# Kernel optimization log

Hardware: AMD Instinct MI355X
Metric: run time of the kernel (lower is better)

The kernel has to match this reference:

```python
import jax, jax.numpy as jnp
import numpy as np


def _rel_coords_log(ws: int) -> np.ndarray:
    # matches torch.meshgrid default indexing='ij'
    idx = np.arange(ws, dtype=np.float32)
    coords = np.stack(np.meshgrid(idx, idx, indexing='ij'), axis=0).reshape(2, -1)  # [2, ws^2]
    rel = coords[:, :, None] - coords[:, None, :]  # [2, T, T]
    rel = rel.transpose(1, 2, 0).reshape(-1, 2)    # [T*T, 2]
    return np.sign(rel) * np.log1p(np.abs(rel))


def setup_inputs() -> dict:
    key = jax.random.key(0)
    ks = jax.random.split(key, 9)
    B, C, Hd, ws, meta_h = 256, 256, 8, 16, 256
    s = 1.0 / np.sqrt(C)
    return {
        'x': jax.random.normal(ks[0], (B, C, ws, ws), dtype=jnp.float32),
        'w_qkv': jax.random.normal(ks[1], (3 * C, C), dtype=jnp.float32) * s,
        'b_qkv': jax.random.normal(ks[2], (3 * C,), dtype=jnp.float32) * 0.01,
        'w_proj': jax.random.normal(ks[3], (C, C), dtype=jnp.float32) * s,
        'b_proj': jax.random.normal(ks[4], (C,), dtype=jnp.float32) * 0.01,
        'mw1': jax.random.normal(ks[5], (meta_h, 2), dtype=jnp.float32) * 0.5,
        'mb1': jax.random.normal(ks[6], (meta_h,), dtype=jnp.float32) * 0.01,
        'mw2': jax.random.normal(ks[7], (Hd, meta_h), dtype=jnp.float32) * (1.0 / np.sqrt(meta_h)),
        'mb2': jax.random.normal(ks[8], (Hd,), dtype=jnp.float32) * 0.01,
        'tau': jnp.ones((1, Hd, 1, 1), dtype=jnp.float32),
    }


def reference(x, w_qkv, b_qkv, w_proj, b_proj, mw1, mb1, mw2, mb2, tau):
    B, C, H, W = x.shape
    T = H * W
    nh = tau.shape[1]
    hd = C // nh
    # [B, C, H, W] -> [B, T, C]
    xt = x.reshape(B, C, T).transpose(0, 2, 1)
    qkv = xt @ w_qkv.T + b_qkv                                  # [B, T, 3C]
    qkv = qkv.reshape(B, T, 3, nh, hd).transpose(2, 0, 3, 1, 4)  # [3, B, nh, T, hd]
    q, k, v = qkv[0], qkv[1], qkv[2]
    # cosine similarity attention
    qn = jnp.linalg.norm(q, axis=-1, keepdims=True)              # [B, nh, T, 1]
    kn = jnp.linalg.norm(k, axis=-1, keepdims=True)
    denom = jnp.maximum(qn * kn.transpose(0, 1, 3, 2), 1e-6)
    scores = jnp.einsum('bhqd,bhkd->bhqk', q, k) / denom
    scores = scores / jnp.maximum(tau, 0.01)
    # MLP relative position bias (static coords)
    rc = jnp.asarray(_rel_coords_log(H))                          # [T*T, 2]
    bias = jax.nn.relu(rc @ mw1.T + mb1) @ mw2.T + mb2            # [T*T, nh]
    bias = bias.T.reshape(nh, T, T)
    scores = scores + bias[None]
    attn = jax.nn.softmax(scores, axis=-1)
    out = jnp.einsum('bhqk,bhkd->bhqd', attn, v)                  # [B, nh, T, hd]
    out = out.transpose(0, 2, 1, 3).reshape(B, T, C)
    out = out @ w_proj.T + b_proj
    return out.transpose(0, 2, 1).reshape(B, C, H, W)
```

## Files before the change

kernel.cpp:

```cpp
#include <hip/hip_runtime.h>
#include <math.h>

#define Cc 256
#define NH 8
#define HD 32
#define Tt 256
#define MH 256
#define TBL 961

typedef _Float16 f16;
typedef f16 f16x4 __attribute__((ext_vector_type(4)));
typedef f16 f16x8 __attribute__((ext_vector_type(8)));
typedef float f32x4 __attribute__((ext_vector_type(4)));

__device__ __forceinline__ f16x8 ld8(const f16* base, int row, int kc) {
  return *(const f16x8*)&base[row * 32 + ((kc ^ ((row >> 2) & 3)) << 3)];
}
__device__ __forceinline__ void st8(f16* base, int row, int kc, f16x8 v) {
  *(f16x8*)&base[row * 32 + ((kc ^ ((row >> 2) & 3)) << 3)] = v;
}
__device__ __forceinline__ int sidx(int row, int col) {
  return row * 32 + (((col >> 3) ^ ((row >> 2) & 3)) << 3) + (col & 7);
}
__device__ __forceinline__ int vsidx(int d, int t) {
  return d * 256 + (((t >> 3) ^ (d & 7)) << 3) + (t & 7);
}
__device__ __forceinline__ f16x8 vld8(const f16* base, int d, int tch) {
  return *(const f16x8*)&base[d * 256 + ((tch ^ (d & 7)) << 3)];
}

__global__ __launch_bounds__(256) void prep_kernel(
    const float* __restrict__ mw1, const float* __restrict__ mb1,
    const float* __restrict__ mw2, const float* __restrict__ mb2,
    const float* __restrict__ w_proj, const float* __restrict__ w_qkv,
    float* __restrict__ table, float* __restrict__ tablemax,
    f16* __restrict__ wpf, f16* __restrict__ wqf) {
  int blk = blockIdx.x, tid = threadIdx.x;
  if (blk >= NH + 32) {
    int blk2 = blk - NH - 32;
#pragma unroll
    for (int pass = 0; pass < 4; pass++) {
      int chunkid = blk2 * 256 + tid + pass * 6144;
      int row = chunkid >> 5, ck = chunkid & 31;
      int hh = row / 96, n = row % 96;
      int srow = ((n >> 5) << 8) + (hh << 5) + (n & 31);
      const float* wp = w_qkv + (size_t)srow * Cc + ck * 8;
      f16x8 v;
#pragma unroll
      for (int u = 0; u < 8; u++) v[u] = (f16)wp[u];
      *(f16x8*)&wqf[(size_t)row * Cc + ck * 8] = v;
    }
    return;
  }
  if (blk >= NH) {
    int base = (blk - NH) * 2048 + tid * 8;
    f16x8 v;
#pragma unroll
    for (int u = 0; u < 8; u++) v[u] = (f16)w_proj[base + u];
    *(f16x8*)&wpf[base] = v;
    return;
  }
  __shared__ float s_w1a[MH], s_w1b[MH], s_b1[MH], s_w2[MH];
  __shared__ float red[256];
  for (int i = tid; i < MH; i += 256) {
    s_w1a[i] = mw1[2 * i];
    s_w1b[i] = mw1[2 * i + 1];
    s_b1[i] = mb1[i];
    s_w2[i] = mw2[blk * MH + i];
  }
  __syncthreads();
  float lmax = -1e30f;
  float b2 = mb2[blk];
  for (int idx = tid; idx < TBL; idx += 256) {
    float fdi = (float)(idx / 31 - 15);
    float fdj = (float)(idx % 31 - 15);
    float d0 = (fdi > 0.f ? 1.f : (fdi < 0.f ? -1.f : 0.f)) * log1pf(fabsf(fdi));
    float d1 = (fdj > 0.f ? 1.f : (fdj < 0.f ? -1.f : 0.f)) * log1pf(fabsf(fdj));
    float o = b2;
    for (int m = 0; m < MH; m++) {
      float hid = fmaxf(fmaf(d0, s_w1a[m], fmaf(d1, s_w1b[m], s_b1[m])), 0.f);
      o = fmaf(hid, s_w2[m], o);
    }
    table[blk * TBL + idx] = o;
    lmax = fmaxf(lmax, o);
  }
  red[tid] = lmax;
  __syncthreads();
  for (int s = 128; s > 0; s >>= 1) {
    if (tid < s) red[tid] = fmaxf(red[tid], red[tid + s]);
    __syncthreads();
  }
  if (tid == 0) tablemax[blk] = red[0];
}

__global__ __launch_bounds__(256) void xpose_kernel(const float* __restrict__ x,
                                                    f16* __restrict__ xt) {
  __shared__ __align__(16) f16 tile[64 * 72];
  int blk = blockIdx.x;
  int b = blk >> 4, ti = (blk >> 2) & 3, tj = blk & 3;
  int tid = threadIdx.x;
  const float* xb = x + (size_t)b * 65536;
  int t4 = (tid & 15) * 4, cg = tid >> 4;
#pragma unroll
  for (int p = 0; p < 4; p++) {
    int cl = cg + p * 16;
    float4 v = *(const float4*)&xb[(size_t)(ti * 64 + cl) * 256 + tj * 64 + t4];
    const float* vp = (const float*)&v;
#pragma unroll
    for (int u = 0; u < 4; u++) {
      int tl = t4 + u;
      tile[tl * 72 + (((cl >> 3) ^ (tl & 7)) << 3) + (cl & 7)] = (f16)vp[u];
    }
  }
  __syncthreads();
  f16* xtb = xt + (size_t)b * 65536;
#pragma unroll
  for (int u = 0; u < 2; u++) {
    int chunk = tid * 2 + u;
    int tr = chunk >> 3, ck = chunk & 7;
    f16x8 v = *(const f16x8*)&tile[tr * 72 + ((ck ^ (tr & 7)) << 3)];
    *(f16x8*)&xtb[(size_t)(tj * 64 + tr) * 256 + ti * 64 + ck * 8] = v;
  }
}

__global__ __launch_bounds__(512, 4) void fused_attn(
    const f16* __restrict__ xt, const f16* __restrict__ wqf,
    const float* __restrict__ b_qkv, const float* __restrict__ table,
    const float* __restrict__ tablemax, const float* __restrict__ tau,
    f16* __restrict__ attnH) {
  __shared__ __align__(16) char smem[68352];
  f16* Qa = (f16*)smem;
  f16* Ka = (f16*)(smem + 16384);
  f16* Vt = (f16*)(smem + 32768);
  f16* Pspare = (f16*)(smem + 49152);
  float* tbv = (float*)(smem + 51456);
  float* rs = (float*)(smem + 67328);
  f16* Xa = (f16*)smem;
  f16* Wa = (f16*)(smem + 16384);

  int tid = threadIdx.x;
  int o = blockIdx.x;
  int bh = ((o & 7) << 8) | (o >> 3);
  int b = bh >> 3, h = bh & 7;
  int wv = tid >> 6, ln = tid & 63, lq = ln >> 4, lm = ln & 15;

  const float LOG2E = 1.4426950408889634f;
  float rtau = 1.0f / fmaxf(tau[h], 0.01f);
  float tmaxh = tablemax[h];

  for (int idx = tid; idx < 31 * 32; idx += 512) {
    int di_ = idx >> 5, c = idx & 31;
    float4 v;
    float* vp = (float*)&v;
#pragma unroll
    for (int u = 0; u < 4; u++) {
      int dj = c - u;
      dj = dj < 0 ? 0 : (dj > 30 ? 30 : dj);
      vp[u] = (table[h * TBL + di_ * 31 + dj] - tmaxh - rtau * 1.0001f) * LOG2E;
    }
    *(float4*)&tbv[idx * 4] = v;
  }

  float bj[6];
#pragma unroll
  for (int nt = 0; nt < 6; nt++) {
    int n = nt * 16 + lm;
    int row = ((n >> 5) << 8) + (h << 5) + (n & 31);
    bj[nt] = b_qkv[row];
  }

  const f16* xtb = xt + (size_t)b * 65536;
  const f16* wqh = wqf + (size_t)h * 24576;
  int xt_ = tid >> 1, xkc = (tid & 1) * 2;
  int wn = tid >> 2, wck = tid & 3;

  f32x4 acc[2][6] = {};
  f16x8 xv0, xv1, wvv;
  xv0 = *(const f16x8*)&xtb[xt_ * 256 + xkc * 8];
  xv1 = *(const f16x8*)&xtb[xt_ * 256 + xkc * 8 + 8];
  if (tid < 384) wvv = *(const f16x8*)&wqh[wn * 256 + wck * 8];

  for (int c0 = 0; c0 < Cc; c0 += 32) {
    st8(Xa, xt_, xkc, xv0);
    st8(Xa, xt_, xkc + 1, xv1);
    if (tid < 384) st8(Wa, wn, wck, wvv);
    __syncthreads();
    if (c0 + 32 < Cc) {
      xv0 = *(const f16x8*)&xtb[xt_ * 256 + c0 + 32 + xkc * 8];
      xv1 = *(const f16x8*)&xtb[xt_ * 256 + c0 + 32 + xkc * 8 + 8];
      if (tid < 384) wvv = *(const f16x8*)&wqh[wn * 256 + c0 + 32 + wck * 8];
    }
    f16x8 af[2], bf[6];
#pragma unroll
    for (int e = 0; e < 2; e++) af[e] = ld8(Xa, wv * 32 + e * 16 + lm, lq);
#pragma unroll
    for (int nt = 0; nt < 6; nt++) bf[nt] = ld8(Wa, nt * 16 + lm, lq);
#pragma unroll
    for (int e = 0; e < 2; e++)
#pragma unroll
      for (int nt = 0; nt < 6; nt++)
        acc[e][nt] = __builtin_amdgcn_mfma_f32_16x16x32_f16(af[e], bf[nt],
                                                            acc[e][nt], 0, 0, 0);
    __syncthreads();
  }

#pragma unroll
  for (int e = 0; e < 2; e++) {
#pragma unroll
    for (int nt = 0; nt < 6; nt++) {
      int d = (nt & 1) * 16 + lm;
#pragma unroll
      for (int r = 0; r < 4; r++) {
        int t = wv * 32 + e * 16 + lq * 4 + r;
        f16 v = (f16)(acc[e][nt][r] + bj[nt]);
        if (nt < 2)      Qa[sidx(t, d)] = v;
        else if (nt < 4) Ka[sidx(t, d)] = v;
        else             Vt[vsidx(d, t)] = v;
      }
    }
  }
  __syncthreads();

  if (tid < 256) {
    int t = tid;
    float s = 0.f;
    f16x8 v[4];
#pragma unroll
    for (int ck = 0; ck < 4; ck++) {
      v[ck] = ld8(Qa, t, ck);
#pragma unroll
      for (int u = 0; u < 8; u++) { float f = (float)v[ck][u]; s = fmaf(f, f, s); }
    }
    float sc_ = rsqrtf(s) * rtau * LOG2E;
#pragma unroll
    for (int ck = 0; ck < 4; ck++) {
      f16x8 o2;
#pragma unroll
      for (int u = 0; u < 8; u++) o2[u] = (f16)((float)v[ck][u] * sc_);
      st8(Qa, t, ck, o2);
    }
  } else {
    int t = tid - 256;
    float s = 0.f;
    f16x8 v[4];
#pragma unroll
    for (int ck = 0; ck < 4; ck++) {
      v[ck] = ld8(Ka, t, ck);
#pragma unroll
      for (int u = 0; u < 8; u++) { float f = (float)v[ck][u]; s = fmaf(f, f, s); }
    }
    float sc_ = rsqrtf(s);
#pragma unroll
    for (int ck = 0; ck < 4; ck++) {
      f16x8 o2;
#pragma unroll
      for (int u = 0; u < 8; u++) o2[u] = (f16)((float)v[ck][u] * sc_);
      st8(Ka, t, ck, o2);
    }
  }
  __syncthreads();

  f16x8 qf[2];
#pragma unroll
  for (int e = 0; e < 2; e++) qf[e] = ld8(Qa, wv * 32 + e * 16 + lm, lq);
  __syncthreads();

  f16* Pme = (wv < 7) ? (Qa + wv * 1152) : Pspare;
  int c0l = lm - lq * 4 + 15;
  const float4* tbp = (const float4*)tbv;
  float lsum[2] = {0.f, 0.f};
  f32x4 acco[2][2] = {};
  int dibase = wv * 2 + 15;

  for (int n0 = 0; n0 < Tt; n0 += 32) {
    f16x8 kf[2];
#pragma unroll
    for (int nt = 0; nt < 2; nt++) kf[nt] = ld8(Ka, n0 + nt * 16 + lm, lq);
    f32x4 zero = {0.f, 0.f, 0.f, 0.f};
    f32x4 sc[2][2];
    __builtin_amdgcn_s_setprio(1);
#pragma unroll
    for (int e = 0; e < 2; e++)
#pragma unroll
      for (int nt = 0; nt < 2; nt++)
        sc[e][nt] = __builtin_amdgcn_mfma_f32_16x16x32_f16(kf[nt], qf[e], zero,
                                                           0, 0, 0);
    __builtin_amdgcn_s_setprio(0);
#pragma unroll
    for (int e = 0; e < 2; e++) {
#pragma unroll
      for (int nt = 0; nt < 2; nt++) {
        int di_ = dibase + e - (n0 >> 4) - nt;
        float4 bv = tbp[di_ * 32 + c0l];
        const float* bvp = (const float*)&bv;
        f16x4 pv;
#pragma unroll
        for (int r = 0; r < 4; r++) {
          float p = exp2f(sc[e][nt][r] + bvp[r]);
          lsum[e] += p;
          pv[r] = (f16)p;
        }
        *(f16x4*)&Pme[(e * 16 + lm) * 36 + nt * 16 + lq * 4] = pv;
      }
    }
    asm volatile("s_waitcnt lgkmcnt(0)" ::: "memory");
    f16x8 pf[2], vf[2];
#pragma unroll
    for (int e = 0; e < 2; e++) {
      f16x4 p0 = *(f16x4*)&Pme[(e * 16 + lm) * 36 + lq * 8];
      f16x4 p1 = *(f16x4*)&Pme[(e * 16 + lm) * 36 + lq * 8 + 4];
      pf[e] = __builtin_shufflevector(p0, p1, 0, 1, 2, 3, 4, 5, 6, 7);
    }
#pragma unroll
    for (int dt = 0; dt < 2; dt++)
      vf[dt] = vld8(Vt, dt * 16 + lm, (n0 >> 3) + lq);
    __builtin_amdgcn_s_setprio(1);
#pragma unroll
    for (int e = 0; e < 2; e++)
#pragma unroll
      for (int dt = 0; dt < 2; dt++)
        acco[e][dt] = __builtin_amdgcn_mfma_f32_16x16x32_f16(pf[e], vf[dt],
                                                             acco[e][dt], 0, 0, 0);
    __builtin_amdgcn_s_setprio(0);
  }

#pragma unroll
  for (int e = 0; e < 2; e++) {
    float v = lsum[e];
    v += __shfl_xor(v, 16);
    v += __shfl_xor(v, 32);
    lsum[e] = v;
  }
  if (ln < 16) {
    rs[wv * 32 + lm] = lsum[0];
    rs[wv * 32 + 16 + lm] = lsum[1];
  }
  asm volatile("s_waitcnt lgkmcnt(0)" ::: "memory");
#pragma unroll
  for (int e = 0; e < 2; e++)
#pragma unroll
    for (int r = 0; r < 4; r++) {
      float rl = __builtin_amdgcn_rcpf(rs[wv * 32 + e * 16 + lq * 4 + r]);
      int q = wv * 32 + e * 16 + lq * 4 + r;
#pragma unroll
      for (int dt = 0; dt < 2; dt++) {
        int d = dt * 16 + lm;
        attnH[((size_t)b * Tt + q) * Cc + h * HD + d] =
            (f16)(acco[e][dt][r] * rl);
      }
    }
}

__global__ __launch_bounds__(256, 4) void proj_gemm(
    const f16* __restrict__ A, const f16* __restrict__ wf,
    const float* __restrict__ bp, float* __restrict__ out) {
  __shared__ __align__(16) f16 Af[128 * 72];
  __shared__ __align__(16) f16 Wsh[128 * 72];
  __shared__ float sB[128];
  int tid = threadIdx.x;
  int row0 = blockIdx.x * 128;
  int n0g = blockIdx.y * 128;
  int b = row0 >> 8, t0 = row0 & 255;
  int wv = tid >> 6, ln = tid & 63, lq = ln >> 4, lm = ln & 15;
  int cw = (wv & 1) * 64, tw = (wv >> 1) * 64;

  if (tid < 128) sB[tid] = bp[n0g + tid];

  f32x4 acc[4][4] = {};
  for (int k0 = 0; k0 < Cc; k0 += 64) {
#pragma unroll
    for (int p = 0; p < 4; p++) {
      int idx = p * 256 + tid;
      int row = idx >> 3, ch = idx & 7;
      f16x8 v = *(const f16x8*)&A[(size_t)(row0 + row) * Cc + k0 + ch * 8];
      *(f16x8*)&Af[row * 72 + ch * 8] = v;
    }
#pragma unroll
    for (int p = 0; p < 4; p++) {
      int idx = p * 256 + tid;
      int row = idx >> 3, ch = idx & 7;
      f16x8 v = *(const f16x8*)&wf[(size_t)(n0g + row) * Cc + k0 + ch * 8];
      *(f16x8*)&Wsh[row * 72 + ch * 8] = v;
    }
    __syncthreads();
#pragma unroll
    for (int kk = 0; kk < 2; kk++) {
      f16x8 wfr[4], af[4];
#pragma unroll
      for (int i = 0; i < 4; i++)
        wfr[i] = *(f16x8*)&Wsh[(cw + i * 16 + lm) * 72 + (kk * 4 + lq) * 8];
#pragma unroll
      for (int j = 0; j < 4; j++)
        af[j] = *(f16x8*)&Af[(tw + j * 16 + lm) * 72 + (kk * 4 + lq) * 8];
#pragma unroll
      for (int i = 0; i < 4; i++)
#pragma unroll
        for (int j = 0; j < 4; j++)
          acc[i][j] = __builtin_amdgcn_mfma_f32_16x16x32_f16(wfr[i], af[j],
                                                             acc[i][j], 0, 0, 0);
    }
    __syncthreads();
  }

#pragma unroll
  for (int i = 0; i < 4; i++)
#pragma unroll
    for (int r = 0; r < 4; r++) {
      int crl = cw + i * 16 + lq * 4 + r;
      float bias = sB[crl];
#pragma unroll
      for (int j = 0; j < 4; j++) {
        int tcl = tw + j * 16 + lm;
        out[(size_t)b * 65536 + (size_t)(n0g + crl) * 256 + t0 + tcl] =
            acc[i][j][r] + bias;
      }
    }
}

extern "C" void kernel_launch(void* const* d_in, const int* in_sizes, int n_in,
                              void* d_out, int out_size, void* d_ws,
                              size_t ws_size, hipStream_t stream) {
  const float* x = (const float*)d_in[0];
  const float* w_qkv = (const float*)d_in[1];
  const float* b_qkv = (const float*)d_in[2];
  const float* w_proj = (const float*)d_in[3];
  const float* b_proj = (const float*)d_in[4];
  const float* mw1 = (const float*)d_in[5];
  const float* mb1 = (const float*)d_in[6];
  const float* mw2 = (const float*)d_in[7];
  const float* mb2 = (const float*)d_in[8];
  const float* tau = (const float*)d_in[9];
  float* out = (float*)d_out;

  const size_t NEEDED = (size_t)(TBL * NH + NH) * 4 + (size_t)65536 * 2 +
                        (size_t)256 * NH * Tt * HD * 2;
  if (ws_size < NEEDED) return;

  float* table = (float*)d_ws;
  float* tablemax = table + TBL * NH;
  f16* wpf = (f16*)(tablemax + NH);
  f16* attnH = wpf + 65536;

  f16* xt = (f16*)d_out;
  f16* wqf = (f16*)d_out + (size_t)256 * 65536;

  prep_kernel<<<64, 256, 0, stream>>>(mw1, mb1, mw2, mb2, w_proj, w_qkv, table,
                                      tablemax, wpf, wqf);
  xpose_kernel<<<4096, 256, 0, stream>>>(x, xt);
  fused_attn<<<256 * NH, 512, 0, stream>>>(xt, wqf, b_qkv, table, tablemax,
                                           tau, attnH);
  dim3 g3(512, 2);
  proj_gemm<<<g3, 256, 0, stream>>>(attnH, wpf, b_proj, out);
}
```

Before: 256.4 us.

## Merge prep and transpose kernels, compute row sums via MFMA

Folds the weight/bias-table prep kernel and the x transpose kernel into a single launch, saving one kernel boundary. The bias MLP loop now processes four table entries per thread, reading packed float4 weights from shared memory. In the attention kernel the softmax row sums come from an extra MFMA against a vector of ones, replacing scalar accumulation plus a shuffle and shared-memory reduction, and V is stored as vectorized f16x4 writes. The extra MFMA sums the f16-rounded probabilities, which changes rounding slightly and adds matrix-core work per tile.

```diff
diff --git a/kernel.cpp b/kernel.cpp
--- a/kernel.cpp
+++ b/kernel.cpp
@@ -29,13 +29,46 @@
   return *(const f16x8*)&base[d * 256 + ((tch ^ (d & 7)) << 3)];
 }
 
-__global__ __launch_bounds__(256) void prep_kernel(
+__global__ __launch_bounds__(256) void stage0_kernel(
+    const float* __restrict__ x, f16* __restrict__ xt,
     const float* __restrict__ mw1, const float* __restrict__ mb1,
     const float* __restrict__ mw2, const float* __restrict__ mb2,
     const float* __restrict__ w_proj, const float* __restrict__ w_qkv,
     float* __restrict__ table, float* __restrict__ tablemax,
     f16* __restrict__ wpf, f16* __restrict__ wqf) {
-  int blk = blockIdx.x, tid = threadIdx.x;
+  __shared__ __align__(16) char smem0[9216];
+  int tid = threadIdx.x;
+  int blk = blockIdx.x;
+
+  if (blk < 4096) {
+    f16* tile = (f16*)smem0;
+    int b = blk >> 4, ti = (blk >> 2) & 3, tj = blk & 3;
+    const float* xb = x + (size_t)b * 65536;
+    int t4 = (tid & 15) * 4, cg = tid >> 4;
+#pragma unroll
+    for (int p = 0; p < 4; p++) {
+      int cl = cg + p * 16;
+      float4 v = *(const float4*)&xb[(size_t)(ti * 64 + cl) * 256 + tj * 64 + t4];
+      const float* vp = (const float*)&v;
+#pragma unroll
+      for (int u = 0; u < 4; u++) {
+        int tl = t4 + u;
+        tile[tl * 72 + (((cl >> 3) ^ (tl & 7)) << 3) + (cl & 7)] = (f16)vp[u];
+      }
+    }
+    __syncthreads();
+    f16* xtb = xt + (size_t)b * 65536;
+#pragma unroll
+    for (int u = 0; u < 2; u++) {
+      int chunk = tid * 2 + u;
+      int tr = chunk >> 3, ck = chunk & 7;
+      f16x8 v = *(const f16x8*)&tile[tr * 72 + ((ck ^ (tr & 7)) << 3)];
+      *(f16x8*)&xtb[(size_t)(tj * 64 + tr) * 256 + ti * 64 + ck * 8] = v;
+    }
+    return;
+  }
+
+  blk -= 4096;
   if (blk >= NH + 32) {
     int blk2 = blk - NH - 32;
 #pragma unroll
@@ -60,29 +93,45 @@
     *(f16x8*)&wpf[base] = v;
     return;
   }
-  __shared__ float s_w1a[MH], s_w1b[MH], s_b1[MH], s_w2[MH];
-  __shared__ float red[256];
+  float4* s_w = (float4*)smem0;
+  float* red = (float*)(smem0 + 4096);
   for (int i = tid; i < MH; i += 256) {
-    s_w1a[i] = mw1[2 * i];
-    s_w1b[i] = mw1[2 * i + 1];
-    s_b1[i] = mb1[i];
-    s_w2[i] = mw2[blk * MH + i];
+    float4 w;
+    w.x = mw1[2 * i];
+    w.y = mw1[2 * i + 1];
+    w.z = mb1[i];
+    w.w = mw2[blk * MH + i];
+    s_w[i] = w;
   }
   __syncthreads();
+  float b2 = mb2[blk];
+  float d0v[4], d1v[4], ov[4];
+#pragma unroll
+  for (int j = 0; j < 4; j++) {
+    int idx = tid + j * 256;
+    int ii = idx < TBL ? idx : TBL - 1;
+    float fdi = (float)(ii / 31 - 15);
+    float fdj = (float)(ii % 31 - 15);
+    d0v[j] = (fdi > 0.f ? 1.f : (fdi < 0.f ? -1.f : 0.f)) * log1pf(fabsf(fdi));
+    d1v[j] = (fdj > 0.f ? 1.f : (fdj < 0.f ? -1.f : 0.f)) * log1pf(fabsf(fdj));
+    ov[j] = b2;
+  }
+  for (int m = 0; m < MH; m++) {
+    float4 w = s_w[m];
+#pragma unroll
+    for (int j = 0; j < 4; j++) {
+      float hid = fmaxf(fmaf(d0v[j], w.x, fmaf(d1v[j], w.y, w.z)), 0.f);
+      ov[j] = fmaf(hid, w.w, ov[j]);
+    }
+  }
   float lmax = -1e30f;
-  float b2 = mb2[blk];
-  for (int idx = tid; idx < TBL; idx += 256) {
-    float fdi = (float)(idx / 31 - 15);
-    float fdj = (float)(idx % 31 - 15);
-    float d0 = (fdi > 0.f ? 1.f : (fdi < 0.f ? -1.f : 0.f)) * log1pf(fabsf(fdi));
-    float d1 = (fdj > 0.f ? 1.f : (fdj < 0.f ? -1.f : 0.f)) * log1pf(fabsf(fdj));
-    float o = b2;
-    for (int m = 0; m < MH; m++) {
-      float hid = fmaxf(fmaf(d0, s_w1a[m], fmaf(d1, s_w1b[m], s_b1[m])), 0.f);
-      o = fmaf(hid, s_w2[m], o);
-    }
-    table[blk * TBL + idx] = o;
-    lmax = fmaxf(lmax, o);
+#pragma unroll
+  for (int j = 0; j < 4; j++) {
+    int idx = tid + j * 256;
+    if (idx < TBL) {
+      table[blk * TBL + idx] = ov[j];
+      lmax = fmaxf(lmax, ov[j]);
+    }
   }
   red[tid] = lmax;
   __syncthreads();
@@ -91,36 +140,6 @@
     __syncthreads();
   }
   if (tid == 0) tablemax[blk] = red[0];
-}
-
-__global__ __launch_bounds__(256) void xpose_kernel(const float* __restrict__ x,
-                                                    f16* __restrict__ xt) {
-  __shared__ __align__(16) f16 tile[64 * 72];
-  int blk = blockIdx.x;
-  int b = blk >> 4, ti = (blk >> 2) & 3, tj = blk & 3;
-  int tid = threadIdx.x;
-  const float* xb = x + (size_t)b * 65536;
-  int t4 = (tid & 15) * 4, cg = tid >> 4;
-#pragma unroll
-  for (int p = 0; p < 4; p++) {
-    int cl = cg + p * 16;
-    float4 v = *(const float4*)&xb[(size_t)(ti * 64 + cl) * 256 + tj * 64 + t4];
-    const float* vp = (const float*)&v;
-#pragma unroll
-    for (int u = 0; u < 4; u++) {
-      int tl = t4 + u;
-      tile[tl * 72 + (((cl >> 3) ^ (tl & 7)) << 3) + (cl & 7)] = (f16)vp[u];
-    }
-  }
-  __syncthreads();
-  f16* xtb = xt + (size_t)b * 65536;
-#pragma unroll
-  for (int u = 0; u < 2; u++) {
-    int chunk = tid * 2 + u;
-    int tr = chunk >> 3, ck = chunk & 7;
-    f16x8 v = *(const f16x8*)&tile[tr * 72 + ((ck ^ (tr & 7)) << 3)];
-    *(f16x8*)&xtb[(size_t)(tj * 64 + tr) * 256 + ti * 64 + ck * 8] = v;
-  }
 }
 
 __global__ __launch_bounds__(512, 4) void fused_attn(
@@ -128,13 +147,12 @@
     const float* __restrict__ b_qkv, const float* __restrict__ table,
     const float* __restrict__ tablemax, const float* __restrict__ tau,
     f16* __restrict__ attnH) {
-  __shared__ __align__(16) char smem[68352];
+  __shared__ __align__(16) char smem[67328];
   f16* Qa = (f16*)smem;
   f16* Ka = (f16*)(smem + 16384);
   f16* Vt = (f16*)(smem + 32768);
   f16* Pspare = (f16*)(smem + 49152);
   float* tbv = (float*)(smem + 51456);
-  float* rs = (float*)(smem + 67328);
   f16* Xa = (f16*)smem;
   f16* Wa = (f16*)(smem + 16384);
 
@@ -209,13 +227,20 @@
 #pragma unroll
     for (int nt = 0; nt < 6; nt++) {
       int d = (nt & 1) * 16 + lm;
-#pragma unroll
-      for (int r = 0; r < 4; r++) {
-        int t = wv * 32 + e * 16 + lq * 4 + r;
-        f16 v = (f16)(acc[e][nt][r] + bj[nt]);
-        if (nt < 2)      Qa[sidx(t, d)] = v;
-        else if (nt < 4) Ka[sidx(t, d)] = v;
-        else             Vt[vsidx(d, t)] = v;
+      if (nt < 4) {
+#pragma unroll
+        for (int r = 0; r < 4; r++) {
+          int t = wv * 32 + e * 16 + lq * 4 + r;
+          f16 v = (f16)(acc[e][nt][r] + bj[nt]);
+          if (nt < 2) Qa[sidx(t, d)] = v;
+          else        Ka[sidx(t, d)] = v;
+        }
+      } else {
+        int t0 = wv * 32 + e * 16 + lq * 4;
+        f16x4 pv;
+#pragma unroll
+        for (int r = 0; r < 4; r++) pv[r] = (f16)(acc[e][nt][r] + bj[nt]);
+        *(f16x4*)&Vt[vsidx(d, t0)] = pv;
       }
     }
   }
@@ -268,8 +293,11 @@
   f16* Pme = (wv < 7) ? (Qa + wv * 1152) : Pspare;
   int c0l = lm - lq * 4 + 15;
   const float4* tbp = (const float4*)tbv;
-  float lsum[2] = {0.f, 0.f};
   f32x4 acco[2][2] = {};
+  f32x4 acco_s[2] = {};
+  f16x8 onev;
+#pragma unroll
+  for (int u = 0; u < 8; u++) onev[u] = (f16)1.0f;
   int dibase = wv * 2 + 15;
 
   for (int n0 = 0; n0 < Tt; n0 += 32) {
@@ -295,11 +323,7 @@
         const float* bvp = (const float*)&bv;
         f16x4 pv;
 #pragma unroll
-        for (int r = 0; r < 4; r++) {
-          float p = exp2f(sc[e][nt][r] + bvp[r]);
-          lsum[e] += p;
-          pv[r] = (f16)p;
-        }
+        for (int r = 0; r < 4; r++) pv[r] = (f16)exp2f(sc[e][nt][r] + bvp[r]);
         *(f16x4*)&Pme[(e * 16 + lm) * 36 + nt * 16 + lq * 4] = pv;
       }
     }
@@ -316,31 +340,22 @@
       vf[dt] = vld8(Vt, dt * 16 + lm, (n0 >> 3) + lq);
     __builtin_amdgcn_s_setprio(1);
 #pragma unroll
-    for (int e = 0; e < 2; e++)
+    for (int e = 0; e < 2; e++) {
 #pragma unroll
       for (int dt = 0; dt < 2; dt++)
         acco[e][dt] = __builtin_amdgcn_mfma_f32_16x16x32_f16(pf[e], vf[dt],
                                                              acco[e][dt], 0, 0, 0);
+      acco_s[e] = __builtin_amdgcn_mfma_f32_16x16x32_f16(pf[e], onev,
+                                                         acco_s[e], 0, 0, 0);
+    }
     __builtin_amdgcn_s_setprio(0);
   }
 
 #pragma unroll
-  for (int e = 0; e < 2; e++) {
-    float v = lsum[e];
-    v += __shfl_xor(v, 16);
-    v += __shfl_xor(v, 32);
-    lsum[e] = v;
-  }
-  if (ln < 16) {
-    rs[wv * 32 + lm] = lsum[0];
-    rs[wv * 32 + 16 + lm] = lsum[1];
-  }
-  asm volatile("s_waitcnt lgkmcnt(0)" ::: "memory");
-#pragma unroll
   for (int e = 0; e < 2; e++)
 #pragma unroll
     for (int r = 0; r < 4; r++) {
-      float rl = __builtin_amdgcn_rcpf(rs[wv * 32 + e * 16 + lq * 4 + r]);
+      float rl = __builtin_amdgcn_rcpf(acco_s[e][r]);
       int q = wv * 32 + e * 16 + lq * 4 + r;
 #pragma unroll
       for (int dt = 0; dt < 2; dt++) {
@@ -444,9 +459,8 @@
   f16* xt = (f16*)d_out;
   f16* wqf = (f16*)d_out + (size_t)256 * 65536;
 
-  prep_kernel<<<64, 256, 0, stream>>>(mw1, mb1, mw2, mb2, w_proj, w_qkv, table,
-                                      tablemax, wpf, wqf);
-  xpose_kernel<<<4096, 256, 0, stream>>>(x, xt);
+  stage0_kernel<<<4160, 256, 0, stream>>>(x, xt, mw1, mb1, mw2, mb2, w_proj,
+                                          w_qkv, table, tablemax, wpf, wqf);
   fused_attn<<<256 * NH, 512, 0, stream>>>(xt, wqf, b_qkv, table, tablemax,
                                            tau, attnH);
   dim3 g3(512, 2);
```

New measurement: 244.7 us. 4.6% less time.
